# Performance work log

Measured on AMD Instinct MI355X. Metric: run time of the kernel, lower is better.

## Reference

```python
import jax, jax.numpy as jnp
import numpy as np
from jax import lax

ALPHA = 2.0  # spikingjelly surrogate.ATan default

@jax.custom_vjp
def atan_spike(x):
    # Heaviside forward, ATan surrogate backward
    return (x >= 0.0).astype(x.dtype)

def _atan_fwd(x):
    return atan_spike(x), x

def _atan_bwd(x, g):
    return (g * (ALPHA / 2.0) / (1.0 + (jnp.pi / 2.0 * ALPHA * x) ** 2),)

atan_spike.defvjp(_atan_fwd, _atan_bwd)

def plif(x_seq, w):
    """ParametricLIFNode, multi-step. init tau=2 -> w=0, decay=sigmoid(w).
    v <- v + (x - (v - v_reset)) * sigmoid(w); hard reset to v_reset=0."""
    decay = jax.nn.sigmoid(w)
    def step(v, x):
        v = v + (x - v) * decay
        s = atan_spike(v - 1.0)  # v_threshold = 1.0
        return v * (1.0 - s), s  # hard reset (v_reset = 0)
    _, s_seq = lax.scan(step, jnp.zeros_like(x_seq[0]), x_seq)
    return s_seq

def conv2d(x, w):
    return lax.conv_general_dilated(x, w, (1, 1), 'VALID',
                                    dimension_numbers=('NCHW', 'OIHW', 'NCHW'))

def bn(x, g, b, eps=1e-5):
    # training-mode BatchNorm2d over the folded (T*B, C, H, W) batch
    m = x.mean(axis=(0, 2, 3), keepdims=True)
    v = x.var(axis=(0, 2, 3), keepdims=True)
    return (x - m) * lax.rsqrt(v + eps) * g.reshape(1, -1, 1, 1) + b.reshape(1, -1, 1, 1)

def maxpool2(x):
    return lax.reduce_window(x, -jnp.inf, lax.max, (1, 1, 2, 2), (1, 1, 2, 2), 'VALID')

def block(x_seq, wc, g, b, wl):
    # conv -> BN (time folded into batch) -> PLIF over time -> maxpool
    T, B = x_seq.shape[0], x_seq.shape[1]
    y = x_seq.reshape((T * B,) + x_seq.shape[2:])
    y = bn(conv2d(y, wc), g, b)
    y = y.reshape((T, B) + y.shape[1:])
    s = plif(y, wl)
    p = maxpool2(s.reshape((T * B,) + s.shape[2:]))
    return p.reshape((T, B) + p.shape[1:])


def setup_inputs() -> dict:
    key = jax.random.key(0)
    ks = jax.random.split(key, 8)
    B, C, H, W = 32, 3, 128, 128

    def cw(k, o, i):
        return (jax.random.normal(k, (o, i, 5, 5), jnp.float32)
                / np.float32(np.sqrt(i * 25)))

    return {
        'x': jax.random.normal(ks[0], (B, C, H, W), jnp.float32),
        'w_conv1': cw(ks[1], 16, 3),
        'w_conv2': cw(ks[2], 32, 16),
        'w_conv3': cw(ks[3], 32, 32),
        'w_conv4': cw(ks[4], 64, 32),
        'gamma1': jnp.ones(16, jnp.float32), 'beta1': jnp.zeros(16, jnp.float32),
        'gamma2': jnp.ones(32, jnp.float32), 'beta2': jnp.zeros(32, jnp.float32),
        'gamma3': jnp.ones(32, jnp.float32), 'beta3': jnp.zeros(32, jnp.float32),
        'gamma4': jnp.ones(64, jnp.float32), 'beta4': jnp.zeros(64, jnp.float32),
        'w_lif1': jnp.zeros((), jnp.float32), 'w_lif2': jnp.zeros((), jnp.float32),
        'w_lif3': jnp.zeros((), jnp.float32), 'w_lif4': jnp.zeros((), jnp.float32),
        'w_lif5': jnp.zeros((), jnp.float32), 'w_lif6': jnp.zeros((), jnp.float32),
        'fc1_w': jax.random.normal(ks[5], (1024, 1024), jnp.float32) / np.float32(32.0),
        'fc1_b': jnp.zeros(1024, jnp.float32),
        'fc2_w': jax.random.normal(ks[6], (10, 1024), jnp.float32) / np.float32(32.0),
        'fc2_b': jnp.zeros(10, jnp.float32),
    }


def reference(x, w_conv1, w_conv2, w_conv3, w_conv4,
              gamma1, beta1, gamma2, beta2, gamma3, beta3, gamma4, beta4,
              w_lif1, w_lif2, w_lif3, w_lif4, w_lif5, w_lif6,
              fc1_w, fc1_b, fc2_w, fc2_b):
    T = 5  # n_steps
    x_seq = jnp.broadcast_to(x[None], (T,) + x.shape)  # repeat over time
    h = block(x_seq, w_conv1, gamma1, beta1, w_lif1)
    h = block(h, w_conv2, gamma2, beta2, w_lif2)
    h = block(h, w_conv3, gamma3, beta3, w_lif3)
    h = block(h, w_conv4, gamma4, beta4, w_lif4)
    Tt, B = h.shape[0], h.shape[1]
    f = h.reshape(Tt, B, -1)  # [T, B, 1024]
    s1 = plif(jnp.einsum('tbf,of->tbo', f, fc1_w) + fc1_b, w_lif5)
    # Dropout(0.5) is identity in eval mode
    s2 = plif(jnp.einsum('tbf,of->tbo', s1, fc2_w) + fc2_b, w_lif6)
    return s2.mean(axis=0)  # firing rate over time [B, 10]
```

## Files before the change

### kernel.cpp

```cpp
#include <hip/hip_runtime.h>
#include <math.h>

#define T_STEPS 5
#define BATCH 32

template <int CIN, int CB, int HIN, int WINP, int HOUT, int WOUT, int TILES_W,
          bool CLAMP, int MINW>
__global__ __launch_bounds__(256, MINW) void conv5_rb(
    const float* __restrict__ in, const float* __restrict__ wgt,
    float* __restrict__ out) {
  __shared__ __align__(16) float wlds[CIN * 25 * CB];
  const int tid = threadIdx.x;
  const int n = blockIdx.z;
  const int cob = blockIdx.y;
  const int Cout = gridDim.y * CB;

  for (int i = tid; i < CIN * 25 * CB; i += 256) {
    int co = i & (CB - 1);
    int k = i / CB;
    wlds[i] = wgt[(cob * CB + co) * (CIN * 25) + k];
  }
  __syncthreads();

  const int cog = tid >> 6;
  const int rg = (tid >> 2) & 15;
  const int cg = tid & 3;
  const int th = blockIdx.x / TILES_W;
  const int twi = blockIdx.x - th * TILES_W;
  const int row0 = th * 32 + rg * 2;
  const int col0 = twi * 16 + cg * 4;

  float acc[4][2][4];
#pragma unroll
  for (int a = 0; a < 4; ++a)
#pragma unroll
    for (int b = 0; b < 2; ++b)
#pragma unroll
      for (int c = 0; c < 4; ++c) acc[a][b][c] = 0.f;

  const float* ip = in + (long)n * CIN * (HIN * WINP) + row0 * WINP + col0;

  for (int ci = 0; ci < CIN; ++ci) {
    float win[6][8];
    if (CLAMP) {
      const float* pp = in + ((long)n * CIN + ci) * (HIN * WINP);
#pragma unroll
      for (int rr = 0; rr < 6; ++rr)
#pragma unroll
        for (int jj = 0; jj < 8; ++jj) {
          int off = (row0 + rr) * WINP + (col0 + jj);
          off = off < HIN * WINP - 1 ? off : HIN * WINP - 1;
          win[rr][jj] = pp[off];
        }
    } else {
#pragma unroll
      for (int rr = 0; rr < 6; ++rr) {
        float4 a4 = *reinterpret_cast<const float4*>(ip + rr * WINP);
        float4 b4 = *reinterpret_cast<const float4*>(ip + rr * WINP + 4);
        win[rr][0] = a4.x; win[rr][1] = a4.y; win[rr][2] = a4.z;
        win[rr][3] = a4.w; win[rr][4] = b4.x; win[rr][5] = b4.y;
        win[rr][6] = b4.z; win[rr][7] = b4.w;
      }
      ip += HIN * WINP;
    }

    const float* wp = &wlds[ci * 25 * CB + cog * 4];
#pragma unroll
    for (int kh = 0; kh < 5; ++kh)
#pragma unroll
      for (int kw = 0; kw < 5; ++kw) {
        float4 wv = *reinterpret_cast<const float4*>(wp + (kh * 5 + kw) * CB);
        float wa[4] = {wv.x, wv.y, wv.z, wv.w};
#pragma unroll
        for (int co = 0; co < 4; ++co)
#pragma unroll
          for (int r2 = 0; r2 < 2; ++r2)
#pragma unroll
            for (int c4 = 0; c4 < 4; ++c4)
              acc[co][r2][c4] =
                  fmaf(win[kh + r2][kw + c4], wa[co], acc[co][r2][c4]);
      }
  }

#pragma unroll
  for (int co = 0; co < 4; ++co) {
    int coG = cob * CB + cog * 4 + co;
    float* op = out + ((long)n * Cout + coG) * (HOUT * WOUT);
#pragma unroll
    for (int r2 = 0; r2 < 2; ++r2) {
      int ho = row0 + r2;
      if (ho < HOUT) {
#pragma unroll
        for (int c4 = 0; c4 < 4; ++c4) {
          int wo = col0 + c4;
          if (wo < WOUT) op[ho * WOUT + wo] = acc[co][r2][c4];
        }
      }
    }
  }
}

__global__ __launch_bounds__(256) void conv4_rb(const float* __restrict__ in,
                                                const float* __restrict__ wgt,
                                                float* __restrict__ out) {
  const int tid = threadIdx.x;
  const int px = tid & 63;
  const int cog = tid >> 6;
  const int cob = blockIdx.x;
  const int n = blockIdx.y;
  const int r = px >> 3, c = px & 7;
  const int co0 = cob * 16 + cog * 4;
  float acc[4] = {0.f, 0.f, 0.f, 0.f};
  const float* ip = in + (long)n * 32 * 144 + r * 12 + c;
  for (int ci = 0; ci < 32; ++ci) {
    float win[5][5];
#pragma unroll
    for (int kh = 0; kh < 5; ++kh)
#pragma unroll
      for (int kw = 0; kw < 5; ++kw) win[kh][kw] = ip[kh * 12 + kw];
    ip += 144;
    const float* wp = wgt + ci * 25;
#pragma unroll
    for (int kk = 0; kk < 25; ++kk) {
#pragma unroll
      for (int j = 0; j < 4; ++j) {
        float w = wp[(co0 + j) * 800 + kk];
        acc[j] = fmaf(win[kk / 5][kk % 5], w, acc[j]);
      }
    }
  }
  float* op = out + ((long)n * 64 + co0) * 64 + px;
#pragma unroll
  for (int j = 0; j < 4; ++j) op[j * 64] = acc[j];
}

__global__ __launch_bounds__(256) void bn_partial(
    const float* __restrict__ y, int C, int M, int HW, double inv_hw,
    double* __restrict__ psum, double* __restrict__ psq, int S) {
  const int c = blockIdx.x / S;
  const int s = blockIdx.x - c * S;
  const int tid = threadIdx.x;
  double sum = 0.0, sumsq = 0.0;
  for (int i = s * 256 + tid; i < M; i += S * 256) {
    int n = (int)((double)i * inv_hw);
    int hw = i - n * HW;
    if (hw < 0) { n--; hw += HW; }
    else if (hw >= HW) { n++; hw -= HW; }
    float v = y[((long)n * C + c) * (long)HW + hw];
    sum += (double)v;
    sumsq += (double)v * (double)v;
  }
  __shared__ double ls[256], ls2[256];
  ls[tid] = sum;
  ls2[tid] = sumsq;
  __syncthreads();
  for (int off = 128; off > 0; off >>= 1) {
    if (tid < off) {
      ls[tid] += ls[tid + off];
      ls2[tid] += ls2[tid + off];
    }
    __syncthreads();
  }
  if (tid == 0) {
    psum[blockIdx.x] = ls[0];
    psq[blockIdx.x] = ls2[0];
  }
}

__global__ void bn_finalize(const double* __restrict__ psum,
                            const double* __restrict__ psq,
                            const float* __restrict__ gamma,
                            const float* __restrict__ beta,
                            float* __restrict__ scale,
                            float* __restrict__ shift, int C, int S,
                            double invM) {
  int c = threadIdx.x;
  if (c >= C) return;
  double s = 0.0, s2 = 0.0;
  for (int i = 0; i < S; ++i) {
    s += psum[c * S + i];
    s2 += psq[c * S + i];
  }
  double m = s * invM;
  double var = s2 * invM - m * m;
  double r = 1.0 / sqrt(var + 1e-5);
  double sc = (double)gamma[c] * r;
  scale[c] = (float)sc;
  shift[c] = (float)((double)beta[c] - m * sc);
}

__global__ __launch_bounds__(256) void plif_pool(
    const float* __restrict__ y, const float* __restrict__ scale,
    const float* __restrict__ shift, const float* __restrict__ wlif,
    float* __restrict__ p, int C, int H, int W, int PH, int PW, int PWp,
    long t_stride) {
  int idx = blockIdx.x * 256 + threadIdx.x;
  int total = BATCH * C * PH * PWp;
  if (idx >= total) return;
  int pw = idx % PWp;
  int t2 = idx / PWp;
  int ph = t2 % PH;
  t2 /= PH;
  int c = t2 % C;
  int b = t2 / C;
  const long pstr = (long)BATCH * C * PH * PWp;
  const long pbase = (((long)b * C + c) * PH + ph) * PWp + pw;
  if (pw >= PW) {
#pragma unroll
    for (int t = 0; t < T_STEPS; ++t) p[t * pstr + pbase] = 0.f;
    return;
  }
  const float sc = scale[c], sh = shift[c];
  const float decay = 1.f / (1.f + expf(-wlif[0]));
  const long base = (((long)b * C + c) * H + 2 * ph) * W + 2 * pw;
  float v0 = 0.f, v1 = 0.f, v2 = 0.f, v3 = 0.f;
#pragma unroll
  for (int t = 0; t < T_STEPS; ++t) {
    const float* yp = y + t * t_stride + base;
    float x0 = yp[0] * sc + sh;
    float x1 = yp[1] * sc + sh;
    float x2 = yp[W] * sc + sh;
    float x3 = yp[W + 1] * sc + sh;
    v0 += (x0 - v0) * decay;
    v1 += (x1 - v1) * decay;
    v2 += (x2 - v2) * decay;
    v3 += (x3 - v3) * decay;
    float s0 = (v0 >= 1.f) ? 1.f : 0.f;
    float s1 = (v1 >= 1.f) ? 1.f : 0.f;
    float s2 = (v2 >= 1.f) ? 1.f : 0.f;
    float s3 = (v3 >= 1.f) ? 1.f : 0.f;
    v0 = (v0 >= 1.f) ? 0.f : v0;
    v1 = (v1 >= 1.f) ? 0.f : v1;
    v2 = (v2 >= 1.f) ? 0.f : v2;
    v3 = (v3 >= 1.f) ? 0.f : v3;
    p[t * pstr + pbase] = fmaxf(fmaxf(s0, s1), fmaxf(s2, s3));
  }
}

__global__ __launch_bounds__(256) void fc_kernel(const float* __restrict__ x,
                                                 const float* __restrict__ w,
                                                 float* __restrict__ out,
                                                 int K, int O, int obpn) {
  int n = blockIdx.x / obpn;
  int o = (blockIdx.x - n * obpn) * 256 + threadIdx.x;
  if (o >= O) return;
  const float4* xr = reinterpret_cast<const float4*>(x + (long)n * K);
  const float4* wr = reinterpret_cast<const float4*>(w + (long)o * K);
  float acc = 0.f;
  for (int k = 0; k < K / 4; ++k) {
    float4 a = xr[k];
    float4 b = wr[k];
    acc += a.x * b.x + a.y * b.y + a.z * b.z + a.w * b.w;
  }
  out[(long)n * O + o] = acc;
}

__global__ __launch_bounds__(256) void plif_fc(const float* __restrict__ h,
                                               const float* __restrict__ bias,
                                               const float* __restrict__ wlif,
                                               float* __restrict__ s_out,
                                               int F) {
  int idx = blockIdx.x * 256 + threadIdx.x;
  if (idx >= BATCH * F) return;
  int f = idx % F;
  int b = idx / F;
  const float decay = 1.f / (1.f + expf(-wlif[0]));
  const float bi = bias[f];
  float v = 0.f;
#pragma unroll
  for (int t = 0; t < T_STEPS; ++t) {
    long off = ((long)(t * BATCH + b)) * F + f;
    float x = h[off] + bi;
    v += (x - v) * decay;
    float s = (v >= 1.f) ? 1.f : 0.f;
    v = (v >= 1.f) ? 0.f : v;
    s_out[off] = s;
  }
}

__global__ __launch_bounds__(256) void plif_mean(const float* __restrict__ h,
                                                 const float* __restrict__ bias,
                                                 const float* __restrict__ wlif,
                                                 float* __restrict__ out,
                                                 int O) {
  int idx = blockIdx.x * 256 + threadIdx.x;
  if (idx >= BATCH * O) return;
  int o = idx % O;
  int b = idx / O;
  const float decay = 1.f / (1.f + expf(-wlif[0]));
  const float bi = bias[o];
  float v = 0.f, sum = 0.f;
#pragma unroll
  for (int t = 0; t < T_STEPS; ++t) {
    float x = h[(long)(t * BATCH + b) * O + o] + bi;
    v += (x - v) * decay;
    float s = (v >= 1.f) ? 1.f : 0.f;
    v = (v >= 1.f) ? 0.f : v;
    sum += s;
  }
  out[(long)b * O + o] = sum / 5.0f;
}

extern "C" void kernel_launch(void* const* d_in, const int* in_sizes, int n_in,
                              void* d_out, int out_size, void* d_ws,
                              size_t ws_size, hipStream_t stream) {
  const float* x = (const float*)d_in[0];
  const float* wc1 = (const float*)d_in[1];
  const float* wc2 = (const float*)d_in[2];
  const float* wc3 = (const float*)d_in[3];
  const float* wc4 = (const float*)d_in[4];
  const float* g1 = (const float*)d_in[5];
  const float* b1 = (const float*)d_in[6];
  const float* g2 = (const float*)d_in[7];
  const float* b2 = (const float*)d_in[8];
  const float* g3 = (const float*)d_in[9];
  const float* b3 = (const float*)d_in[10];
  const float* g4 = (const float*)d_in[11];
  const float* b4 = (const float*)d_in[12];
  const float* wl1 = (const float*)d_in[13];
  const float* wl2 = (const float*)d_in[14];
  const float* wl3 = (const float*)d_in[15];
  const float* wl4 = (const float*)d_in[16];
  const float* wl5 = (const float*)d_in[17];
  const float* wl6 = (const float*)d_in[18];
  const float* fc1w = (const float*)d_in[19];
  const float* fc1b = (const float*)d_in[20];
  const float* fc2w = (const float*)d_in[21];
  const float* fc2b = (const float*)d_in[22];
  float* out = (float*)d_out;

  char* ws = (char*)d_ws;
  float* Y = (float*)ws;
  float* P = (float*)(ws + 68894720);
  char* Sb = ws + 68894720 + 40632320;
  double* psum = (double*)Sb;
  double* psq = psum + 64 * 32;
  float* scale = (float*)(psq + 64 * 32);
  float* shift = scale + 64;

  const int S = 32;

  conv5_rb<3, 16, 128, 128, 124, 124, 8, true, 4>
      <<<dim3(4 * 8, 1, 32), 256, 0, stream>>>(x, wc1, Y);
  {
    int HW = 124 * 124, M = 32 * HW;
    bn_partial<<<16 * S, 256, 0, stream>>>(Y, 16, M, HW, 1.0 / HW, psum, psq, S);
    bn_finalize<<<1, 64, 0, stream>>>(psum, psq, g1, b1, scale, shift, 16, S,
                                      1.0 / (double)M);
  }
  {
    int total = BATCH * 16 * 62 * 64;
    plif_pool<<<(total + 255) / 256, 256, 0, stream>>>(
        Y, scale, shift, wl1, P, 16, 124, 124, 62, 62, 64, 0L);
  }

  conv5_rb<16, 16, 62, 64, 58, 58, 4, false, 4>
      <<<dim3(2 * 4, 2, 160), 256, 0, stream>>>(P, wc2, Y);
  {
    int HW = 58 * 58, M = 160 * HW;
    bn_partial<<<32 * S, 256, 0, stream>>>(Y, 32, M, HW, 1.0 / HW, psum, psq, S);
    bn_finalize<<<1, 64, 0, stream>>>(psum, psq, g2, b2, scale, shift, 32, S,
                                      1.0 / (double)M);
  }
  {
    int total = BATCH * 32 * 29 * 32;
    plif_pool<<<(total + 255) / 256, 256, 0, stream>>>(
        Y, scale, shift, wl2, P, 32, 58, 58, 29, 29, 32,
        (long)BATCH * 32 * 58 * 58);
  }

  conv5_rb<32, 16, 29, 32, 25, 25, 2, false, 3>
      <<<dim3(1 * 2, 2, 160), 256, 0, stream>>>(P, wc3, Y);
  {
    int HW = 25 * 25, M = 160 * HW;
    bn_partial<<<32 * S, 256, 0, stream>>>(Y, 32, M, HW, 1.0 / HW, psum, psq, S);
    bn_finalize<<<1, 64, 0, stream>>>(psum, psq, g3, b3, scale, shift, 32, S,
                                      1.0 / (double)M);
  }
  {
    int total = BATCH * 32 * 12 * 12;
    plif_pool<<<(total + 255) / 256, 256, 0, stream>>>(
        Y, scale, shift, wl3, P, 32, 25, 25, 12, 12, 12,
        (long)BATCH * 32 * 25 * 25);
  }

  conv4_rb<<<dim3(4, 160), 256, 0, stream>>>(P, wc4, Y);
  {
    int HW = 8 * 8, M = 160 * HW;
    bn_partial<<<64 * S, 256, 0, stream>>>(Y, 64, M, HW, 1.0 / HW, psum, psq, S);
    bn_finalize<<<1, 64, 0, stream>>>(psum, psq, g4, b4, scale, shift, 64, S,
                                      1.0 / (double)M);
  }
  {
    int total = BATCH * 64 * 4 * 4;
    plif_pool<<<(total + 255) / 256, 256, 0, stream>>>(
        Y, scale, shift, wl4, P, 64, 8, 8, 4, 4, 4, (long)BATCH * 64 * 8 * 8);
  }

  float* h1 = Y;
  float* s1 = P;
  float* h2 = Y + 163840;
  fc_kernel<<<160 * 4, 256, 0, stream>>>(P, fc1w, h1, 1024, 1024, 4);
  plif_fc<<<(BATCH * 1024 + 255) / 256, 256, 0, stream>>>(h1, fc1b, wl5, s1,
                                                          1024);
  fc_kernel<<<160 * 1, 256, 0, stream>>>(s1, fc2w, h2, 1024, 10, 1);
  plif_mean<<<(BATCH * 10 + 255) / 256, 256, 0, stream>>>(h2, fc2b, wl6, out,
                                                          10);
}
```

Before: 907.2 us.

## Double-buffer conv input windows, stage conv4 weights in LDS, tile fc1 over batch

The conv kernels now prefetch the next input channel's window into a second register buffer while computing on the current one, with sched_barriers to keep the loads ahead of the FMAs. The clamped scalar-load path for conv1 is replaced by clamped row and column indices so it can also use float4 loads. conv4 now stages its weights in LDS and reads them as float4 instead of strided global loads, and fc1 reuses each weight row across 8 batch rows held in shared memory. Launch bounds drop to 2 waves per SIMD, which lowers the occupancy target and raises register use.

Result: slower. 1.225 ms (+35.0%).

```diff
diff --git a/kernel.cpp b/kernel.cpp
--- a/kernel.cpp
+++ b/kernel.cpp
@@ -4,9 +4,45 @@
 #define T_STEPS 5
 #define BATCH 32
 
-template <int CIN, int CB, int HIN, int WINP, int HOUT, int WOUT, int TILES_W,
-          bool CLAMP, int MINW>
-__global__ __launch_bounds__(256, MINW) void conv5_rb(
+template <int WINP, int HIN>
+__device__ __forceinline__ void load_win6x8(float (&w)[6][8],
+                                            const float* __restrict__ plane,
+                                            int row0, int col0) {
+#pragma unroll
+  for (int rr = 0; rr < 6; ++rr) {
+    int r = row0 + rr;
+    r = r < HIN - 1 ? r : HIN - 1;
+    const float* ip = plane + r * WINP + col0;
+    float4 a4 = *reinterpret_cast<const float4*>(ip);
+    float4 b4 = *reinterpret_cast<const float4*>(ip + 4);
+    w[rr][0] = a4.x; w[rr][1] = a4.y; w[rr][2] = a4.z; w[rr][3] = a4.w;
+    w[rr][4] = b4.x; w[rr][5] = b4.y; w[rr][6] = b4.z; w[rr][7] = b4.w;
+  }
+}
+
+template <int CB>
+__device__ __forceinline__ void fma_win(const float (&win)[6][8],
+                                        const float* __restrict__ wp,
+                                        float (&acc)[4][2][4]) {
+#pragma unroll
+  for (int kh = 0; kh < 5; ++kh)
+#pragma unroll
+    for (int kw = 0; kw < 5; ++kw) {
+      float4 wv = *reinterpret_cast<const float4*>(wp + (kh * 5 + kw) * CB);
+      float wa[4] = {wv.x, wv.y, wv.z, wv.w};
+#pragma unroll
+      for (int co = 0; co < 4; ++co)
+#pragma unroll
+        for (int r2 = 0; r2 < 2; ++r2)
+#pragma unroll
+          for (int c4 = 0; c4 < 4; ++c4)
+            acc[co][r2][c4] =
+                fmaf(win[kh + r2][kw + c4], wa[co], acc[co][r2][c4]);
+    }
+}
+
+template <int CIN, int CB, int HIN, int WINP, int HOUT, int WOUT, int TILES_W>
+__global__ __launch_bounds__(256, 2) void conv5_rb(
     const float* __restrict__ in, const float* __restrict__ wgt,
     float* __restrict__ out) {
   __shared__ __align__(16) float wlds[CIN * 25 * CB];
@@ -28,7 +64,8 @@
   const int th = blockIdx.x / TILES_W;
   const int twi = blockIdx.x - th * TILES_W;
   const int row0 = th * 32 + rg * 2;
-  const int col0 = twi * 16 + cg * 4;
+  const int col0r = twi * 16 + cg * 4;
+  const int col0 = col0r < WINP - 8 ? col0r : WINP - 8;
 
   float acc[4][2][4];
 #pragma unroll
@@ -38,48 +75,22 @@
 #pragma unroll
       for (int c = 0; c < 4; ++c) acc[a][b][c] = 0.f;
 
-  const float* ip = in + (long)n * CIN * (HIN * WINP) + row0 * WINP + col0;
-
-  for (int ci = 0; ci < CIN; ++ci) {
-    float win[6][8];
-    if (CLAMP) {
-      const float* pp = in + ((long)n * CIN + ci) * (HIN * WINP);
-#pragma unroll
-      for (int rr = 0; rr < 6; ++rr)
-#pragma unroll
-        for (int jj = 0; jj < 8; ++jj) {
-          int off = (row0 + rr) * WINP + (col0 + jj);
-          off = off < HIN * WINP - 1 ? off : HIN * WINP - 1;
-          win[rr][jj] = pp[off];
-        }
-    } else {
-#pragma unroll
-      for (int rr = 0; rr < 6; ++rr) {
-        float4 a4 = *reinterpret_cast<const float4*>(ip + rr * WINP);
-        float4 b4 = *reinterpret_cast<const float4*>(ip + rr * WINP + 4);
-        win[rr][0] = a4.x; win[rr][1] = a4.y; win[rr][2] = a4.z;
-        win[rr][3] = a4.w; win[rr][4] = b4.x; win[rr][5] = b4.y;
-        win[rr][6] = b4.z; win[rr][7] = b4.w;
-      }
-      ip += HIN * WINP;
-    }
-
-    const float* wp = &wlds[ci * 25 * CB + cog * 4];
-#pragma unroll
-    for (int kh = 0; kh < 5; ++kh)
-#pragma unroll
-      for (int kw = 0; kw < 5; ++kw) {
-        float4 wv = *reinterpret_cast<const float4*>(wp + (kh * 5 + kw) * CB);
-        float wa[4] = {wv.x, wv.y, wv.z, wv.w};
-#pragma unroll
-        for (int co = 0; co < 4; ++co)
-#pragma unroll
-          for (int r2 = 0; r2 < 2; ++r2)
-#pragma unroll
-            for (int c4 = 0; c4 < 4; ++c4)
-              acc[co][r2][c4] =
-                  fmaf(win[kh + r2][kw + c4], wa[co], acc[co][r2][c4]);
-      }
+  const int HW = HIN * WINP;
+  const float* plane = in + (long)n * CIN * HW;
+
+  float A[6][8], Bf[6][8];
+  load_win6x8<WINP, HIN>(A, plane, row0, col0);
+  for (int ci = 0; ci < CIN; ci += 2) {
+    if (ci + 1 < CIN) load_win6x8<WINP, HIN>(Bf, plane + HW, row0, col0);
+    __builtin_amdgcn_sched_barrier(0);
+    fma_win<CB>(A, &wlds[ci * 25 * CB + cog * 4], acc);
+    if (ci + 1 < CIN) {
+      if (ci + 2 < CIN)
+        load_win6x8<WINP, HIN>(A, plane + 2 * HW, row0, col0);
+      __builtin_amdgcn_sched_barrier(0);
+      fma_win<CB>(Bf, &wlds[(ci + 1) * 25 * CB + cog * 4], acc);
+    }
+    plane += 2 * HW;
   }
 
 #pragma unroll
@@ -92,7 +103,7 @@
       if (ho < HOUT) {
 #pragma unroll
         for (int c4 = 0; c4 < 4; ++c4) {
-          int wo = col0 + c4;
+          int wo = col0r + c4;
           if (wo < WOUT) op[ho * WOUT + wo] = acc[co][r2][c4];
         }
       }
@@ -100,36 +111,59 @@
   }
 }
 
-__global__ __launch_bounds__(256) void conv4_rb(const float* __restrict__ in,
-                                                const float* __restrict__ wgt,
-                                                float* __restrict__ out) {
+__device__ __forceinline__ void load_win25(float (&w)[25],
+                                           const float* __restrict__ ip) {
+#pragma unroll
+  for (int kh = 0; kh < 5; ++kh)
+#pragma unroll
+    for (int kw = 0; kw < 5; ++kw) w[kh * 5 + kw] = ip[kh * 12 + kw];
+}
+
+__device__ __forceinline__ void fma_win25(const float (&win)[25],
+                                          const float* __restrict__ wp,
+                                          float (&acc)[4]) {
+#pragma unroll
+  for (int kk = 0; kk < 25; ++kk) {
+    float4 wv = *reinterpret_cast<const float4*>(wp + kk * 16);
+    acc[0] = fmaf(win[kk], wv.x, acc[0]);
+    acc[1] = fmaf(win[kk], wv.y, acc[1]);
+    acc[2] = fmaf(win[kk], wv.z, acc[2]);
+    acc[3] = fmaf(win[kk], wv.w, acc[3]);
+  }
+}
+
+__global__ __launch_bounds__(256, 2) void conv4_rb(
+    const float* __restrict__ in, const float* __restrict__ wgt,
+    float* __restrict__ out) {
+  __shared__ __align__(16) float wlds[32 * 25 * 16];
   const int tid = threadIdx.x;
+  const int cob = blockIdx.x;
+  const int n = blockIdx.y;
+  for (int i = tid; i < 32 * 25 * 16; i += 256) {
+    int co = i & 15;
+    int k = i >> 4;
+    wlds[i] = wgt[(cob * 16 + co) * 800 + k];
+  }
+  __syncthreads();
   const int px = tid & 63;
   const int cog = tid >> 6;
-  const int cob = blockIdx.x;
-  const int n = blockIdx.y;
   const int r = px >> 3, c = px & 7;
-  const int co0 = cob * 16 + cog * 4;
   float acc[4] = {0.f, 0.f, 0.f, 0.f};
   const float* ip = in + (long)n * 32 * 144 + r * 12 + c;
-  for (int ci = 0; ci < 32; ++ci) {
-    float win[5][5];
-#pragma unroll
-    for (int kh = 0; kh < 5; ++kh)
-#pragma unroll
-      for (int kw = 0; kw < 5; ++kw) win[kh][kw] = ip[kh * 12 + kw];
-    ip += 144;
-    const float* wp = wgt + ci * 25;
-#pragma unroll
-    for (int kk = 0; kk < 25; ++kk) {
-#pragma unroll
-      for (int j = 0; j < 4; ++j) {
-        float w = wp[(co0 + j) * 800 + kk];
-        acc[j] = fmaf(win[kk / 5][kk % 5], w, acc[j]);
-      }
-    }
-  }
-  float* op = out + ((long)n * 64 + co0) * 64 + px;
+  float A[25], Bf[25];
+  load_win25(A, ip);
+  for (int ci = 0; ci < 32; ci += 2) {
+    if (ci + 1 < 32) load_win25(Bf, ip + 144);
+    __builtin_amdgcn_sched_barrier(0);
+    fma_win25(A, &wlds[ci * 25 * 16 + cog * 4], acc);
+    if (ci + 1 < 32) {
+      if (ci + 2 < 32) load_win25(A, ip + 288);
+      __builtin_amdgcn_sched_barrier(0);
+      fma_win25(Bf, &wlds[(ci + 1) * 25 * 16 + cog * 4], acc);
+    }
+    ip += 288;
+  }
+  float* op = out + ((long)n * 64 + cob * 16 + cog * 4) * 64 + px;
 #pragma unroll
   for (int j = 0; j < 4; ++j) op[j * 64] = acc[j];
 }
@@ -235,6 +269,32 @@
     v3 = (v3 >= 1.f) ? 0.f : v3;
     p[t * pstr + pbase] = fmaxf(fmaxf(s0, s1), fmaxf(s2, s3));
   }
+}
+
+__global__ __launch_bounds__(256, 2) void fc1_tiled(
+    const float* __restrict__ x, const float* __restrict__ w,
+    float* __restrict__ out) {
+  __shared__ __align__(16) float xs[8][1024];
+  const int tid = threadIdx.x;
+  const int n0 = blockIdx.y * 8;
+  const int o = blockIdx.x * 256 + tid;
+  for (int i = tid; i < 8 * 1024; i += 256) {
+    int nn = i >> 10, k = i & 1023;
+    xs[nn][k] = x[(long)(n0 + nn) * 1024 + k];
+  }
+  __syncthreads();
+  const float4* wr = reinterpret_cast<const float4*>(w + (long)o * 1024);
+  float acc[8] = {0.f, 0.f, 0.f, 0.f, 0.f, 0.f, 0.f, 0.f};
+  for (int k4 = 0; k4 < 256; ++k4) {
+    float4 w4 = wr[k4];
+#pragma unroll
+    for (int nn = 0; nn < 8; ++nn) {
+      float4 xv = *reinterpret_cast<const float4*>(&xs[nn][k4 * 4]);
+      acc[nn] += w4.x * xv.x + w4.y * xv.y + w4.z * xv.z + w4.w * xv.w;
+    }
+  }
+#pragma unroll
+  for (int nn = 0; nn < 8; ++nn) out[(long)(n0 + nn) * 1024 + o] = acc[nn];
 }
 
 __global__ __launch_bounds__(256) void fc_kernel(const float* __restrict__ x,
@@ -340,7 +400,7 @@
 
   const int S = 32;
 
-  conv5_rb<3, 16, 128, 128, 124, 124, 8, true, 4>
+  conv5_rb<3, 16, 128, 128, 124, 124, 8>
       <<<dim3(4 * 8, 1, 32), 256, 0, stream>>>(x, wc1, Y);
   {
     int HW = 124 * 124, M = 32 * HW;
@@ -354,7 +414,7 @@
         Y, scale, shift, wl1, P, 16, 124, 124, 62, 62, 64, 0L);
   }
 
-  conv5_rb<16, 16, 62, 64, 58, 58, 4, false, 4>
+  conv5_rb<16, 16, 62, 64, 58, 58, 4>
       <<<dim3(2 * 4, 2, 160), 256, 0, stream>>>(P, wc2, Y);
   {
     int HW = 58 * 58, M = 160 * HW;
@@ -369,7 +429,7 @@
         (long)BATCH * 32 * 58 * 58);
   }
 
-  conv5_rb<32, 16, 29, 32, 25, 25, 2, false, 3>
+  conv5_rb<32, 16, 29, 32, 25, 25, 2>
       <<<dim3(1 * 2, 2, 160), 256, 0, stream>>>(P, wc3, Y);
   {
     int HW = 25 * 25, M = 160 * HW;
@@ -400,7 +460,7 @@
   float* h1 = Y;
   float* s1 = P;
   float* h2 = Y + 163840;
-  fc_kernel<<<160 * 4, 256, 0, stream>>>(P, fc1w, h1, 1024, 1024, 4);
+  fc1_tiled<<<dim3(4, 20), 256, 0, stream>>>(P, fc1w, h1);
   plif_fc<<<(BATCH * 1024 + 255) / 256, 256, 0, stream>>>(h1, fc1b, wl5, s1,
                                                           1024);
   fc_kernel<<<160 * 1, 256, 0, stream>>>(s1, fc2w, h2, 1024, 10, 1);
```
